# Optimization experiments

Hardware: AMD Instinct MI355X
Metric: run time of the kernel (lower is better)

## Reference

```python
import jax, jax.numpy as jnp
import numpy as np

D_MODEL = 2048
NUM_HEADS = 16
D_HEAD = D_MODEL // NUM_HEADS
ROPE_THETA = 10000.0
MAX_SEQ_LEN = 2048
NEG_INF = -1e30


def _rope_tables(seq_len):
    pos = jnp.arange(seq_len, dtype=jnp.float32)[:, None]          # [s,1]
    i = jnp.arange(0, D_HEAD, 2, dtype=jnp.float32)                 # [d/2]
    freqs = 1.0 / (ROPE_THETA ** (i / D_HEAD))
    angles = pos * freqs                                            # [s, d/2]
    return jnp.cos(angles), jnp.sin(angles)


def _apply_rope(x, cos, sin):
    # x: [b,h,s,d]; interleaved pairs: x1 = even dims, x2 = odd dims
    x1 = x[..., 0::2]
    x2 = x[..., 1::2]
    r1 = x1 * cos - x2 * sin
    r2 = x1 * sin + x2 * cos
    return jnp.stack([r1, r2], axis=-1).reshape(x.shape)


def setup_inputs() -> dict:
    key = jax.random.key(0)
    ks = jax.random.split(key, 5)
    b, s = 2, 2048
    scale = 1.0 / np.sqrt(D_MODEL)  # ~kaiming fan_in scale
    return {
        "x": jax.random.normal(ks[0], (b, s, D_MODEL), jnp.float32),
        "Wq": jax.random.normal(ks[1], (D_MODEL, D_MODEL), jnp.float32) * scale,
        "bq": jnp.zeros((D_MODEL,), jnp.float32),
        "Wk": jax.random.normal(ks[2], (D_MODEL, D_MODEL), jnp.float32) * scale,
        "bk": jnp.zeros((D_MODEL,), jnp.float32),
        "Wv": jax.random.normal(ks[3], (D_MODEL, D_MODEL), jnp.float32) * scale,
        "bv": jnp.zeros((D_MODEL,), jnp.float32),
        "Wo": jax.random.normal(ks[4], (D_MODEL, D_MODEL), jnp.float32) * scale,
        "bo": jnp.zeros((D_MODEL,), jnp.float32),
    }


def reference(x, Wq, bq, Wk, bk, Wv, bv, Wo, bo):
    b, s, _ = x.shape
    # QKV projections (torch Linear: y = x @ W.T + b)
    q = x @ Wq.T + bq
    k = x @ Wk.T + bk
    v = x @ Wv.T + bv
    # split heads: b s (h d) -> b h s d
    def split(t):
        return t.reshape(b, s, NUM_HEADS, D_HEAD).transpose(0, 2, 1, 3)
    q, k, v = split(q), split(k), split(v)
    # RoPE
    cos, sin = _rope_tables(s)
    q = _apply_rope(q, cos, sin)
    k = _apply_rope(k, cos, sin)
    # scaled dot-product attention with causal mask
    scores = jnp.einsum('bhqd,bhkd->bhqk', q, k) / jnp.sqrt(jnp.float32(D_HEAD))
    causal = jnp.tril(jnp.ones((s, s), dtype=bool))
    scores = jnp.where(causal[None, None], scores, NEG_INF)
    attn = jax.nn.softmax(scores, axis=-1)
    out = jnp.einsum('bhqk,bhkd->bhqd', attn, v)
    # merge heads and output projection
    out = out.transpose(0, 2, 1, 3).reshape(b, s, D_MODEL)
    return out @ Wo.T + bo
```

## Files before the change

### kernel.cpp

```cpp
#include <hip/hip_runtime.h>
#include <math.h>

#define D_MODEL 2048
#define NH 16
#define DH 128
#define SEQ 2048
#define NBH 32

typedef unsigned short u16;
typedef unsigned int u32;
typedef __attribute__((ext_vector_type(8))) short short8;
typedef __attribute__((ext_vector_type(4))) float floatx4;
typedef __attribute__((ext_vector_type(4))) unsigned short ushort4v;

__device__ __forceinline__ u16 f2bf(float f) {
  u32 u = __builtin_bit_cast(u32, f);
  return (u16)((u + 0x8000u) >> 16);
}
__device__ __forceinline__ float bf2f(u16 h) {
  return __builtin_bit_cast(float, (u32)h << 16);
}

__device__ __forceinline__ void async_load16(const u16* g, u16* l) {
  __builtin_amdgcn_global_load_lds(
      (const __attribute__((address_space(1))) void*)g,
      (__attribute__((address_space(3))) void*)l, 16, 0, 0);
}

template <int CTRL>
__device__ __forceinline__ float dpp_mov(float x) {
  return __builtin_bit_cast(
      float, __builtin_amdgcn_update_dpp(0, __builtin_bit_cast(int, x), CTRL,
                                         0xf, 0xf, false));
}
__device__ __forceinline__ float rmax16(float x) {
  x = fmaxf(x, dpp_mov<0x121>(x));
  x = fmaxf(x, dpp_mov<0x122>(x));
  x = fmaxf(x, dpp_mov<0x124>(x));
  x = fmaxf(x, dpp_mov<0x128>(x));
  return x;
}
__device__ __forceinline__ float radd16(float x) {
  x += dpp_mov<0x121>(x);
  x += dpp_mov<0x122>(x);
  x += dpp_mov<0x124>(x);
  x += dpp_mov<0x128>(x);
  return x;
}

__global__ void cvt_multi(const float* __restrict__ s0, u16* __restrict__ d0,
                          const float* __restrict__ s1, u16* __restrict__ d1,
                          const float* __restrict__ s2, u16* __restrict__ d2,
                          const float* __restrict__ s3, u16* __restrict__ d3,
                          const float* __restrict__ s4, u16* __restrict__ d4,
                          int nx, int nw) {
  const float* s;
  u16* d;
  int n;
  switch (blockIdx.y) {
    case 0: s = s0; d = d0; n = nx; break;
    case 1: s = s1; d = d1; n = nw; break;
    case 2: s = s2; d = d2; n = nw; break;
    case 3: s = s3; d = d3; n = nw; break;
    default: s = s4; d = d4; n = nw; break;
  }
  const int i = (blockIdx.x * 256 + threadIdx.x) * 8;
  if (i >= n) return;
  const floatx4 a = *(const floatx4*)(s + i);
  const floatx4 b = *(const floatx4*)(s + i + 4);
  short8 h;
  h[0] = (short)f2bf(a[0]); h[1] = (short)f2bf(a[1]);
  h[2] = (short)f2bf(a[2]); h[3] = (short)f2bf(a[3]);
  h[4] = (short)f2bf(b[0]); h[5] = (short)f2bf(b[1]);
  h[6] = (short)f2bf(b[2]); h[7] = (short)f2bf(b[3]);
  *(short8*)(d + i) = h;
}

__global__ __launch_bounds__(256, 2) void gemm_async(
    const u16* __restrict__ A, const u16* __restrict__ W0,
    const u16* __restrict__ W1, const u16* __restrict__ W2,
    const float* __restrict__ b0, const float* __restrict__ b1,
    const float* __restrict__ b2, void* __restrict__ C0, void* __restrict__ C1,
    void* __restrict__ C2, const int qkv) {
  __shared__ u16 As[128 * 64];
  __shared__ u16 Bs[128 * 64];
  const int tid = threadIdx.x;
  const int wave = tid >> 6, lane = tid & 63;
  const int lr = lane & 15, lg = lane >> 4;
  const int m0 = blockIdx.y * 128;
  const int wm = (wave & 1) * 64, wn = (wave >> 1) * 64;

  int n0, mode;
  const u16* W;
  const float* bias;
  void* C;
  if (qkv) {
    const int which = blockIdx.x >> 4;
    n0 = (blockIdx.x & 15) * 128;
    W = which == 0 ? W0 : which == 1 ? W1 : W2;
    bias = which == 0 ? b0 : which == 1 ? b1 : b2;
    C = which == 0 ? C0 : which == 1 ? C1 : C2;
    mode = which;
  } else {
    n0 = blockIdx.x * 128;
    W = W0; bias = b0; C = C0; mode = 3;
  }

  floatx4 acc[4][4];
#pragma unroll
  for (int i = 0; i < 4; ++i)
#pragma unroll
    for (int j = 0; j < 4; ++j) {
      floatx4 z = {0.f, 0.f, 0.f, 0.f};
      acc[i][j] = z;
    }

  for (int kt = 0; kt < D_MODEL; kt += 64) {
#pragma unroll
    for (int p = 0; p < 4; ++p) {
      const int s = p * 256 + tid;
      const int row = s >> 3, c = s & 7;
      const int g = c ^ (row & 7);
      async_load16(A + (size_t)(m0 + row) * D_MODEL + kt + g * 8,
                   &As[(p * 256 + wave * 64) * 8]);
    }
#pragma unroll
    for (int p = 0; p < 4; ++p) {
      const int s = p * 256 + tid;
      const int row = s >> 3, c = s & 7;
      const int g = c ^ (row & 7);
      async_load16(W + (size_t)(n0 + row) * D_MODEL + kt + g * 8,
                   &Bs[(p * 256 + wave * 64) * 8]);
    }
    __syncthreads();

#pragma unroll
    for (int ks = 0; ks < 2; ++ks) {
      short8 af[4], bfr[4];
      const int ch = (ks * 4 + lg) ^ (lr & 7);
#pragma unroll
      for (int i = 0; i < 4; ++i)
        af[i] = *(const short8*)&As[(wm + 16 * i + lr) * 64 + ch * 8];
#pragma unroll
      for (int j = 0; j < 4; ++j)
        bfr[j] = *(const short8*)&Bs[(wn + 16 * j + lr) * 64 + ch * 8];
#pragma unroll
      for (int i = 0; i < 4; ++i)
#pragma unroll
        for (int j = 0; j < 4; ++j)
          acc[i][j] = __builtin_amdgcn_mfma_f32_16x16x32_bf16(af[i], bfr[j],
                                                              acc[i][j], 0, 0, 0);
    }
    __syncthreads();
  }

  float bj[4];
  int ncol[4];
#pragma unroll
  for (int j = 0; j < 4; ++j) {
    ncol[j] = n0 + wn + 16 * j + lr;
    bj[j] = bias[ncol[j]];
  }

  if (mode == 3) {
    float* Cf = (float*)C;
#pragma unroll
    for (int i = 0; i < 4; ++i)
#pragma unroll
      for (int r = 0; r < 4; ++r) {
        const int m = m0 + wm + 16 * i + lg * 4 + r;
#pragma unroll
        for (int j = 0; j < 4; ++j)
          Cf[(size_t)m * D_MODEL + ncol[j]] = acc[i][j][r] + bj[j];
      }
  } else if (mode == 2) {
    u16* Ch = (u16*)C;
#pragma unroll
    for (int i = 0; i < 4; ++i)
#pragma unroll
      for (int r = 0; r < 4; ++r) {
        const int m = m0 + wm + 16 * i + lg * 4 + r;
        const int b = m >> 11, s = m & (SEQ - 1);
#pragma unroll
        for (int j = 0; j < 4; ++j) {
          const int h = ncol[j] >> 7, d = ncol[j] & (DH - 1);
          Ch[((size_t)((b * NH + h) * DH + d)) * SEQ + s] =
              f2bf(acc[i][j][r] + bj[j]);
        }
      }
  } else {
    u16* Ch = (u16*)C;
#pragma unroll
    for (int i = 0; i < 4; ++i)
#pragma unroll
      for (int r = 0; r < 4; ++r) {
        const int m = m0 + wm + 16 * i + lg * 4 + r;
        const int b = m >> 11, s = m & (SEQ - 1);
#pragma unroll
        for (int j = 0; j < 4; ++j) {
          const int h = ncol[j] >> 7, d = ncol[j] & (DH - 1);
          Ch[((size_t)((b * NH + h) * SEQ + s)) * DH + d] =
              f2bf(acc[i][j][r] + bj[j]);
        }
      }
  }
}

__global__ void rope_kernel(u16* __restrict__ Q, u16* __restrict__ K) {
  const int idx = blockIdx.x * blockDim.x + threadIdx.x;
  const int p = idx & 63;
  const int s = (idx >> 6) & (SEQ - 1);
  const int bh = idx >> 17;
  if (bh >= NBH) return;
  const float freq = exp2f(-(float)p * (13.287712379549449f / 64.0f));
  const float ang = (float)s * freq;
  float sn, cs;
  sincosf(ang, &sn, &cs);
  const size_t base = ((size_t)bh * SEQ + s) * DH + 2 * p;
  {
    const u32 qq = *(const u32*)(Q + base);
    const float x1 = bf2f((u16)(qq & 0xffffu)), x2 = bf2f((u16)(qq >> 16));
    *(u32*)(Q + base) =
        (u32)f2bf(x1 * cs - x2 * sn) | ((u32)f2bf(x1 * sn + x2 * cs) << 16);
  }
  {
    const u32 kk = *(const u32*)(K + base);
    const float x1 = bf2f((u16)(kk & 0xffffu)), x2 = bf2f((u16)(kk >> 16));
    *(u32*)(K + base) =
        (u32)f2bf(x1 * cs - x2 * sn) | ((u32)f2bf(x1 * sn + x2 * cs) << 16);
  }
}

__global__ __launch_bounds__(512, 4) void attn_kernel(
    const u16* __restrict__ Q, const u16* __restrict__ K,
    const u16* __restrict__ Vt, u16* __restrict__ Oflat) {
  __shared__ u16 Ks[64 * 128];
  __shared__ u16 Vts[128 * 64];
  __shared__ u16 Ps[8 * 16 * 72];
  const int tid = threadIdx.x;
  const int wave = tid >> 6, lane = tid & 63;
  const int lr = lane & 15, lg = lane >> 4;
  const int bh = blockIdx.y;
  const int qt = (blockIdx.y < 16) ? blockIdx.x : (15 - blockIdx.x);
  const size_t qk0 = (size_t)bh * SEQ * DH;
  const int q0 = qt * 128 + wave * 16;
  const float SL2E = 0.08838834764831845f * 1.4426950408889634f;

  short8 qf[4];
#pragma unroll
  for (int kb = 0; kb < 4; ++kb)
    qf[kb] = *(const short8*)(Q + qk0 + (size_t)(q0 + lr) * DH + kb * 32 + lg * 8);

  floatx4 o[8];
#pragma unroll
  for (int jd = 0; jd < 8; ++jd) {
    floatx4 z = {0.f, 0.f, 0.f, 0.f};
    o[jd] = z;
  }
  float mrun[4], lrun[4];
#pragma unroll
  for (int r = 0; r < 4; ++r) {
    mrun[r] = -1e38f;
    lrun[r] = 0.f;
  }

  u16* myP = &Ps[wave * 16 * 72];
  const int nkt = 2 * qt + 2;
  for (int kt = 0; kt < nkt; ++kt) {
#pragma unroll
    for (int p = 0; p < 2; ++p) {
      const int s = p * 512 + tid;
      const int row = s >> 4, c = s & 15;
      const int g = c ^ (row & 15);
      async_load16(K + qk0 + (size_t)(kt * 64 + row) * DH + g * 8,
                   &Ks[(p * 512 + wave * 64) * 8]);
    }
#pragma unroll
    for (int p = 0; p < 2; ++p) {
      const int s = p * 512 + tid;
      const int row = s >> 3, c = s & 7;
      const int g = c ^ (row & 7);
      async_load16(Vt + (size_t)bh * DH * SEQ + (size_t)row * SEQ + kt * 64 + g * 8,
                   &Vts[(p * 512 + wave * 64) * 8]);
    }
    __syncthreads();

    floatx4 sacc[4];
#pragma unroll
    for (int j = 0; j < 4; ++j) {
      floatx4 z = {0.f, 0.f, 0.f, 0.f};
      sacc[j] = z;
    }
#pragma unroll
    for (int kb = 0; kb < 4; ++kb) {
      short8 kf[4];
#pragma unroll
      for (int j = 0; j < 4; ++j)
        kf[j] = *(const short8*)&Ks[(16 * j + lr) * 128 + ((kb * 4 + lg) ^ lr) * 8];
#pragma unroll
      for (int j = 0; j < 4; ++j)
        sacc[j] = __builtin_amdgcn_mfma_f32_16x16x32_bf16(qf[kb], kf[j],
                                                          sacc[j], 0, 0, 0);
    }

    const bool mask_tile = (kt >= 2 * qt);
#pragma unroll
    for (int j = 0; j < 4; ++j)
#pragma unroll
      for (int r = 0; r < 4; ++r) {
        float v = sacc[j][r] * SL2E;
        if (mask_tile) {
          const int kpos = kt * 64 + 16 * j + lr;
          const int qpos = q0 + lg * 4 + r;
          if (kpos > qpos) v = -1e30f;
        }
        sacc[j][r] = v;
      }

    float mnew[4], alpha[4], rs[4];
#pragma unroll
    for (int r = 0; r < 4; ++r) {
      float mx = fmaxf(fmaxf(sacc[0][r], sacc[1][r]),
                       fmaxf(sacc[2][r], sacc[3][r]));
      mx = rmax16(mx);
      const float mn = fmaxf(mrun[r], mx);
      mnew[r] = mn;
      alpha[r] = exp2f(mrun[r] - mn);
      mrun[r] = mn;
      rs[r] = 0.f;
    }

#pragma unroll
    for (int j = 0; j < 4; ++j)
#pragma unroll
      for (int r = 0; r < 4; ++r) {
        const float pv = exp2f(sacc[j][r] - mnew[r]);
        rs[r] += pv;
        myP[(lg * 4 + r) * 72 + 16 * j + lr] = f2bf(pv);
      }

#pragma unroll
    for (int r = 0; r < 4; ++r)
      lrun[r] = lrun[r] * alpha[r] + radd16(rs[r]);

#pragma unroll
    for (int jd = 0; jd < 8; ++jd)
#pragma unroll
      for (int r = 0; r < 4; ++r) o[jd][r] *= alpha[r];

    asm volatile("s_waitcnt lgkmcnt(0)" ::: "memory");

#pragma unroll
    for (int kb = 0; kb < 2; ++kb) {
      const short8 pf = *(const short8*)&myP[lr * 72 + kb * 32 + lg * 8];
#pragma unroll
      for (int jd = 0; jd < 8; ++jd) {
        const short8 vf = *(const short8*)&Vts[(16 * jd + lr) * 64 +
                                               ((kb * 4 + lg) ^ (lr & 7)) * 8];
        o[jd] = __builtin_amdgcn_mfma_f32_16x16x32_bf16(pf, vf, o[jd], 0, 0, 0);
      }
    }
    __syncthreads();
  }

  const int b = bh >> 4, h = bh & (NH - 1);
#pragma unroll
  for (int r = 0; r < 4; ++r) {
    const int qpos = q0 + lg * 4 + r;
    const float inv = 1.0f / lrun[r];
    u16* dst = Oflat + ((size_t)(b * SEQ + qpos)) * D_MODEL + h * DH;
#pragma unroll
    for (int jd = 0; jd < 8; ++jd) dst[16 * jd + lr] = f2bf(o[jd][r] * inv);
  }
}

template <int ABF16>
__global__ __launch_bounds__(256, 2) void gemm_kernel(
    const void* __restrict__ Aptr, const float* __restrict__ W,
    const float* __restrict__ bias, void* __restrict__ Cptr, const int mode) {
  __shared__ u16 As[128 * 72];
  __shared__ u16 Bs[128 * 72];
  const int tid = threadIdx.x;
  const int wave = tid >> 6, lane = tid & 63;
  const int lr = lane & 15, lg = lane >> 4;
  const int m0 = blockIdx.y * 128, n0 = blockIdx.x * 128;
  const int wm = (wave & 1) * 64, wn = (wave >> 1) * 64;

  floatx4 acc[4][4];
#pragma unroll
  for (int i = 0; i < 4; ++i)
#pragma unroll
    for (int j = 0; j < 4; ++j) {
      floatx4 z = {0.f, 0.f, 0.f, 0.f};
      acc[i][j] = z;
    }

  for (int kt = 0; kt < D_MODEL; kt += 64) {
    if (ABF16) {
      const u16* A = (const u16*)Aptr;
      const int row0 = tid >> 3, c8 = (tid & 7) * 8;
#pragma unroll
      for (int p = 0; p < 4; ++p) {
        const int row = row0 + p * 32;
        *(short8*)&As[row * 72 + c8] =
            *(const short8*)(A + (size_t)(m0 + row) * D_MODEL + kt + c8);
      }
    } else {
      const float* A = (const float*)Aptr;
      const int row0 = tid >> 4, c4 = (tid & 15) * 4;
#pragma unroll
      for (int p = 0; p < 8; ++p) {
        const int row = row0 + p * 16;
        const floatx4 v =
            *(const floatx4*)(A + (size_t)(m0 + row) * D_MODEL + kt + c4);
        ushort4v h;
        h[0] = f2bf(v[0]); h[1] = f2bf(v[1]); h[2] = f2bf(v[2]); h[3] = f2bf(v[3]);
        *(ushort4v*)&As[row * 72 + c4] = h;
      }
    }
    {
      const int row0 = tid >> 4, c4 = (tid & 15) * 4;
#pragma unroll
      for (int p = 0; p < 8; ++p) {
        const int row = row0 + p * 16;
        const floatx4 v =
            *(const floatx4*)(W + (size_t)(n0 + row) * D_MODEL + kt + c4);
        ushort4v h;
        h[0] = f2bf(v[0]); h[1] = f2bf(v[1]); h[2] = f2bf(v[2]); h[3] = f2bf(v[3]);
        *(ushort4v*)&Bs[row * 72 + c4] = h;
      }
    }
    __syncthreads();
#pragma unroll
    for (int ks = 0; ks < 2; ++ks) {
      short8 af[4], bfr[4];
#pragma unroll
      for (int i = 0; i < 4; ++i)
        af[i] = *(const short8*)&As[(wm + 16 * i + lr) * 72 + ks * 32 + lg * 8];
#pragma unroll
      for (int j = 0; j < 4; ++j)
        bfr[j] = *(const short8*)&Bs[(wn + 16 * j + lr) * 72 + ks * 32 + lg * 8];
#pragma unroll
      for (int i = 0; i < 4; ++i)
#pragma unroll
        for (int j = 0; j < 4; ++j)
          acc[i][j] = __builtin_amdgcn_mfma_f32_16x16x32_bf16(af[i], bfr[j],
                                                              acc[i][j], 0, 0, 0);
    }
    __syncthreads();
  }

  float bj[4];
  int ncol[4];
#pragma unroll
  for (int j = 0; j < 4; ++j) {
    ncol[j] = n0 + wn + 16 * j + lr;
    bj[j] = bias[ncol[j]];
  }

  if (mode == 3) {
    float* C = (float*)Cptr;
#pragma unroll
    for (int i = 0; i < 4; ++i)
#pragma unroll
      for (int r = 0; r < 4; ++r) {
        const int m = m0 + wm + 16 * i + lg * 4 + r;
#pragma unroll
        for (int j = 0; j < 4; ++j)
          C[(size_t)m * D_MODEL + ncol[j]] = acc[i][j][r] + bj[j];
      }
  } else if (mode == 2) {
    u16* C = (u16*)Cptr;
#pragma unroll
    for (int i = 0; i < 4; ++i)
#pragma unroll
      for (int r = 0; r < 4; ++r) {
        const int m = m0 + wm + 16 * i + lg * 4 + r;
        const int b = m >> 11, s = m & (SEQ - 1);
#pragma unroll
        for (int j = 0; j < 4; ++j) {
          const int h = ncol[j] >> 7, d = ncol[j] & (DH - 1);
          C[((size_t)((b * NH + h) * DH + d)) * SEQ + s] = f2bf(acc[i][j][r] + bj[j]);
        }
      }
  } else {
    u16* C = (u16*)Cptr;
#pragma unroll
    for (int i = 0; i < 4; ++i)
#pragma unroll
      for (int r = 0; r < 4; ++r) {
        const int m = m0 + wm + 16 * i + lg * 4 + r;
        const int b = m >> 11, s = m & (SEQ - 1);
#pragma unroll
        for (int j = 0; j < 4; ++j) {
          const int h = ncol[j] >> 7, d = ncol[j] & (DH - 1);
          C[((size_t)((b * NH + h) * SEQ + s)) * DH + d] = f2bf(acc[i][j][r] + bj[j]);
        }
      }
  }
}

extern "C" void kernel_launch(void* const* d_in, const int* in_sizes, int n_in,
                              void* d_out, int out_size, void* d_ws,
                              size_t ws_size, hipStream_t stream) {
  const float* x = (const float*)d_in[0];
  const float* Wq = (const float*)d_in[1];
  const float* bq = (const float*)d_in[2];
  const float* Wk = (const float*)d_in[3];
  const float* bk = (const float*)d_in[4];
  const float* Wv = (const float*)d_in[5];
  const float* bv = (const float*)d_in[6];
  const float* Wo = (const float*)d_in[7];
  const float* bo = (const float*)d_in[8];
  float* out = (float*)d_out;

  const size_t E = (size_t)NBH * SEQ * DH;
  const size_t WE = (size_t)D_MODEL * D_MODEL;
  const size_t need = (4 * E + 4 * WE) * sizeof(u16);

  const dim3 gb(256);

  if (ws_size >= need) {
    u16* xb = (u16*)d_ws;
    u16* wqb = xb + E;
    u16* wkb = wqb + WE;
    u16* wvb = wkb + WE;
    u16* wob = wvb + WE;
    u16* q = wob + WE;
    u16* k = q + E;
    u16* vt = k + E;
    u16* aflat = xb;

    cvt_multi<<<dim3((int)(E / 2048), 5), gb, 0, stream>>>(
        x, xb, Wq, wqb, Wk, wkb, Wv, wvb, Wo, wob, (int)E, (int)WE);

    gemm_async<<<dim3(48, 32), gb, 0, stream>>>(xb, wqb, wkb, wvb, bq, bk, bv,
                                                q, k, vt, 1);
    rope_kernel<<<dim3((NBH * SEQ * (DH / 2)) / 256), gb, 0, stream>>>(q, k);
    attn_kernel<<<dim3(SEQ / 128, NBH), dim3(512), 0, stream>>>(q, k, vt, aflat);
    gemm_async<<<dim3(16, 32), gb, 0, stream>>>(aflat, wob, nullptr, nullptr,
                                                bo, nullptr, nullptr, out,
                                                nullptr, nullptr, 0);
  } else {
    u16* q = (u16*)d_ws;
    u16* k = q + E;
    u16* vt = k + E;
    u16* aflat = vt + E;
    const dim3 gg(D_MODEL / 128, (2 * SEQ) / 128);
    gemm_kernel<0><<<gg, gb, 0, stream>>>(x, Wq, bq, q, 0);
    gemm_kernel<0><<<gg, gb, 0, stream>>>(x, Wk, bk, k, 1);
    gemm_kernel<0><<<gg, gb, 0, stream>>>(x, Wv, bv, vt, 2);
    rope_kernel<<<dim3((NBH * SEQ * (DH / 2)) / 256), dim3(256), 0, stream>>>(q, k);
    attn_kernel<<<dim3(SEQ / 128, NBH), dim3(512), 0, stream>>>(q, k, vt, aflat);
    gemm_kernel<1><<<gg, gb, 0, stream>>>(aflat, Wo, bo, out, 3);
  }
}
```

Baseline: 417.2 us.

## Double-buffer shared tiles in QKV GEMM and attention to overlap loads

The QKV/output GEMM and the attention kernel now keep two shared-memory buffers and prefetch the next K-tile while computing on the current one, with one barrier per iteration instead of two. In attention, the probability tile reuses the consumed K buffer with an XOR swizzle, so extra LDS is avoided and an extra barrier is placed after QK. RoPE switches to the fast __sincosf intrinsic. The cost is double the LDS in the GEMM, which may reduce occupancy, and lower sincos accuracy at large angles.

```diff
diff --git a/kernel.cpp b/kernel.cpp
--- a/kernel.cpp
+++ b/kernel.cpp
@@ -82,8 +82,8 @@
     const float* __restrict__ b0, const float* __restrict__ b1,
     const float* __restrict__ b2, void* __restrict__ C0, void* __restrict__ C1,
     void* __restrict__ C2, const int qkv) {
-  __shared__ u16 As[128 * 64];
-  __shared__ u16 Bs[128 * 64];
+  __shared__ u16 As[2][128 * 64];
+  __shared__ u16 Bs[2][128 * 64];
   const int tid = threadIdx.x;
   const int wave = tid >> 6, lane = tid & 63;
   const int lr = lane & 15, lg = lane >> 4;
@@ -106,23 +106,14 @@
     W = W0; bias = b0; C = C0; mode = 3;
   }
 
-  floatx4 acc[4][4];
-#pragma unroll
-  for (int i = 0; i < 4; ++i)
-#pragma unroll
-    for (int j = 0; j < 4; ++j) {
-      floatx4 z = {0.f, 0.f, 0.f, 0.f};
-      acc[i][j] = z;
-    }
-
-  for (int kt = 0; kt < D_MODEL; kt += 64) {
+  auto stage = [&](int kt, int bsel) {
 #pragma unroll
     for (int p = 0; p < 4; ++p) {
       const int s = p * 256 + tid;
       const int row = s >> 3, c = s & 7;
       const int g = c ^ (row & 7);
       async_load16(A + (size_t)(m0 + row) * D_MODEL + kt + g * 8,
-                   &As[(p * 256 + wave * 64) * 8]);
+                   &As[bsel][(p * 256 + wave * 64) * 8]);
     }
 #pragma unroll
     for (int p = 0; p < 4; ++p) {
@@ -130,9 +121,24 @@
       const int row = s >> 3, c = s & 7;
       const int g = c ^ (row & 7);
       async_load16(W + (size_t)(n0 + row) * D_MODEL + kt + g * 8,
-                   &Bs[(p * 256 + wave * 64) * 8]);
-    }
+                   &Bs[bsel][(p * 256 + wave * 64) * 8]);
+    }
+  };
+
+  floatx4 acc[4][4];
+#pragma unroll
+  for (int i = 0; i < 4; ++i)
+#pragma unroll
+    for (int j = 0; j < 4; ++j) {
+      floatx4 z = {0.f, 0.f, 0.f, 0.f};
+      acc[i][j] = z;
+    }
+
+  stage(0, 0);
+  for (int it = 0; it < 32; ++it) {
+    const int cur = it & 1;
     __syncthreads();
+    if (it < 31) stage((it + 1) * 64, cur ^ 1);
 
 #pragma unroll
     for (int ks = 0; ks < 2; ++ks) {
@@ -140,10 +146,10 @@
       const int ch = (ks * 4 + lg) ^ (lr & 7);
 #pragma unroll
       for (int i = 0; i < 4; ++i)
-        af[i] = *(const short8*)&As[(wm + 16 * i + lr) * 64 + ch * 8];
+        af[i] = *(const short8*)&As[cur][(wm + 16 * i + lr) * 64 + ch * 8];
 #pragma unroll
       for (int j = 0; j < 4; ++j)
-        bfr[j] = *(const short8*)&Bs[(wn + 16 * j + lr) * 64 + ch * 8];
+        bfr[j] = *(const short8*)&Bs[cur][(wn + 16 * j + lr) * 64 + ch * 8];
 #pragma unroll
       for (int i = 0; i < 4; ++i)
 #pragma unroll
@@ -151,7 +157,6 @@
           acc[i][j] = __builtin_amdgcn_mfma_f32_16x16x32_bf16(af[i], bfr[j],
                                                               acc[i][j], 0, 0, 0);
     }
-    __syncthreads();
   }
 
   float bj[4];
@@ -215,7 +220,7 @@
   const float freq = exp2f(-(float)p * (13.287712379549449f / 64.0f));
   const float ang = (float)s * freq;
   float sn, cs;
-  sincosf(ang, &sn, &cs);
+  __sincosf(ang, &sn, &cs);
   const size_t base = ((size_t)bh * SEQ + s) * DH + 2 * p;
   {
     const u32 qq = *(const u32*)(Q + base);
@@ -234,9 +239,8 @@
 __global__ __launch_bounds__(512, 4) void attn_kernel(
     const u16* __restrict__ Q, const u16* __restrict__ K,
     const u16* __restrict__ Vt, u16* __restrict__ Oflat) {
-  __shared__ u16 Ks[64 * 128];
-  __shared__ u16 Vts[128 * 64];
-  __shared__ u16 Ps[8 * 16 * 72];
+  __shared__ u16 Ks[2][64 * 128];
+  __shared__ u16 Vts[2][128 * 64];
   const int tid = threadIdx.x;
   const int wave = tid >> 6, lane = tid & 63;
   const int lr = lane & 15, lg = lane >> 4;
@@ -246,44 +250,56 @@
   const int q0 = qt * 128 + wave * 16;
   const float SL2E = 0.08838834764831845f * 1.4426950408889634f;
 
-  short8 qf[4];
-#pragma unroll
-  for (int kb = 0; kb < 4; ++kb)
-    qf[kb] = *(const short8*)(Q + qk0 + (size_t)(q0 + lr) * DH + kb * 32 + lg * 8);
-
-  floatx4 o[8];
-#pragma unroll
-  for (int jd = 0; jd < 8; ++jd) {
-    floatx4 z = {0.f, 0.f, 0.f, 0.f};
-    o[jd] = z;
-  }
-  float mrun[4], lrun[4];
-#pragma unroll
-  for (int r = 0; r < 4; ++r) {
-    mrun[r] = -1e38f;
-    lrun[r] = 0.f;
-  }
-
-  u16* myP = &Ps[wave * 16 * 72];
-  const int nkt = 2 * qt + 2;
-  for (int kt = 0; kt < nkt; ++kt) {
+  auto stage_k = [&](int kt, int b) {
 #pragma unroll
     for (int p = 0; p < 2; ++p) {
       const int s = p * 512 + tid;
       const int row = s >> 4, c = s & 15;
       const int g = c ^ (row & 15);
       async_load16(K + qk0 + (size_t)(kt * 64 + row) * DH + g * 8,
-                   &Ks[(p * 512 + wave * 64) * 8]);
-    }
+                   &Ks[b][(p * 512 + wave * 64) * 8]);
+    }
+  };
+  auto stage_v = [&](int kt, int b) {
 #pragma unroll
     for (int p = 0; p < 2; ++p) {
       const int s = p * 512 + tid;
       const int row = s >> 3, c = s & 7;
       const int g = c ^ (row & 7);
-      async_load16(Vt + (size_t)bh * DH * SEQ + (size_t)row * SEQ + kt * 64 + g * 8,
-                   &Vts[(p * 512 + wave * 64) * 8]);
-    }
+      async_load16(
+          Vt + (size_t)bh * DH * SEQ + (size_t)row * SEQ + kt * 64 + g * 8,
+          &Vts[b][(p * 512 + wave * 64) * 8]);
+    }
+  };
+
+  short8 qf[4];
+#pragma unroll
+  for (int kb = 0; kb < 4; ++kb)
+    qf[kb] = *(const short8*)(Q + qk0 + (size_t)(q0 + lr) * DH + kb * 32 + lg * 8);
+
+  floatx4 o[8];
+#pragma unroll
+  for (int jd = 0; jd < 8; ++jd) {
+    floatx4 z = {0.f, 0.f, 0.f, 0.f};
+    o[jd] = z;
+  }
+  float mrun[4], lrun[4];
+#pragma unroll
+  for (int r = 0; r < 4; ++r) {
+    mrun[r] = -1e38f;
+    lrun[r] = 0.f;
+  }
+
+  const int nkt = 2 * qt + 2;
+  stage_k(0, 0);
+  stage_v(0, 0);
+  for (int kt = 0; kt < nkt; ++kt) {
+    const int cur = kt & 1;
     __syncthreads();
+    if (kt + 1 < nkt) {
+      stage_k(kt + 1, cur ^ 1);
+      stage_v(kt + 1, cur ^ 1);
+    }
 
     floatx4 sacc[4];
 #pragma unroll
@@ -296,12 +312,16 @@
       short8 kf[4];
 #pragma unroll
       for (int j = 0; j < 4; ++j)
-        kf[j] = *(const short8*)&Ks[(16 * j + lr) * 128 + ((kb * 4 + lg) ^ lr) * 8];
+        kf[j] =
+            *(const short8*)&Ks[cur][(16 * j + lr) * 128 + ((kb * 4 + lg) ^ lr) * 8];
 #pragma unroll
       for (int j = 0; j < 4; ++j)
         sacc[j] = __builtin_amdgcn_mfma_f32_16x16x32_bf16(qf[kb], kf[j],
                                                           sacc[j], 0, 0, 0);
     }
+
+    asm volatile("s_waitcnt lgkmcnt(0)\n\ts_barrier" ::: "memory");
+    u16* myP = &Ks[cur][wave * 1024];
 
     const bool mask_tile = (kt >= 2 * qt);
 #pragma unroll
@@ -336,7 +356,9 @@
       for (int r = 0; r < 4; ++r) {
         const float pv = exp2f(sacc[j][r] - mnew[r]);
         rs[r] += pv;
-        myP[(lg * 4 + r) * 72 + 16 * j + lr] = f2bf(pv);
+        const int row = lg * 4 + r;
+        myP[row * 64 + ((2 * j + (lr >> 3)) ^ (row & 7)) * 8 + (lr & 7)] =
+            f2bf(pv);
       }
 
 #pragma unroll
@@ -352,15 +374,15 @@
 
 #pragma unroll
     for (int kb = 0; kb < 2; ++kb) {
-      const short8 pf = *(const short8*)&myP[lr * 72 + kb * 32 + lg * 8];
+      const short8 pf =
+          *(const short8*)&myP[lr * 64 + ((kb * 4 + lg) ^ (lr & 7)) * 8];
 #pragma unroll
       for (int jd = 0; jd < 8; ++jd) {
-        const short8 vf = *(const short8*)&Vts[(16 * jd + lr) * 64 +
-                                               ((kb * 4 + lg) ^ (lr & 7)) * 8];
+        const short8 vf = *(const short8*)&Vts[cur][(16 * jd + lr) * 64 +
+                                                    ((kb * 4 + lg) ^ (lr & 7)) * 8];
         o[jd] = __builtin_amdgcn_mfma_f32_16x16x32_bf16(pf, vf, o[jd], 0, 0, 0);
       }
     }
-    __syncthreads();
   }
 
   const int b = bh >> 4, h = bh & (NH - 1);
```

New measurement: 457.9 us. +9.7%, slower.

## Shrink attention query tile to 64 rows with 4 waves and swizzled P buffer

Applied to the files above, without the earlier changes.

The attention kernel now uses 256-thread blocks covering 64 query rows instead of 512 threads covering 128. This halves the K/V tile reuse per block but gives finer causal work granularity, twice as many blocks, and only one masked diagonal tile per block. The P scratch buffer moves from padded rows to an XOR-swizzled layout to avoid LDS bank conflicts. RoPE also switches to the fast __sincosf intrinsic, which is less accurate for large angles.

```diff
diff --git a/kernel.cpp b/kernel.cpp
--- a/kernel.cpp
+++ b/kernel.cpp
@@ -215,7 +215,7 @@
   const float freq = exp2f(-(float)p * (13.287712379549449f / 64.0f));
   const float ang = (float)s * freq;
   float sn, cs;
-  sincosf(ang, &sn, &cs);
+  __sincosf(ang, &sn, &cs);
   const size_t base = ((size_t)bh * SEQ + s) * DH + 2 * p;
   {
     const u32 qq = *(const u32*)(Q + base);
@@ -231,19 +231,19 @@
   }
 }
 
-__global__ __launch_bounds__(512, 4) void attn_kernel(
+__global__ __launch_bounds__(256, 4) void attn_kernel(
     const u16* __restrict__ Q, const u16* __restrict__ K,
     const u16* __restrict__ Vt, u16* __restrict__ Oflat) {
   __shared__ u16 Ks[64 * 128];
   __shared__ u16 Vts[128 * 64];
-  __shared__ u16 Ps[8 * 16 * 72];
+  __shared__ u16 Ps[4 * 16 * 64];
   const int tid = threadIdx.x;
   const int wave = tid >> 6, lane = tid & 63;
   const int lr = lane & 15, lg = lane >> 4;
   const int bh = blockIdx.y;
-  const int qt = (blockIdx.y < 16) ? blockIdx.x : (15 - blockIdx.x);
+  const int qt = (bh < 16) ? blockIdx.x : (31 - blockIdx.x);
   const size_t qk0 = (size_t)bh * SEQ * DH;
-  const int q0 = qt * 128 + wave * 16;
+  const int q0 = qt * 64 + wave * 16;
   const float SL2E = 0.08838834764831845f * 1.4426950408889634f;
 
   short8 qf[4];
@@ -264,24 +264,25 @@
     lrun[r] = 0.f;
   }
 
-  u16* myP = &Ps[wave * 16 * 72];
-  const int nkt = 2 * qt + 2;
+  u16* myP = &Ps[wave * 1024];
+  const int nkt = qt + 1;
   for (int kt = 0; kt < nkt; ++kt) {
 #pragma unroll
-    for (int p = 0; p < 2; ++p) {
-      const int s = p * 512 + tid;
+    for (int p = 0; p < 4; ++p) {
+      const int s = p * 256 + tid;
       const int row = s >> 4, c = s & 15;
       const int g = c ^ (row & 15);
       async_load16(K + qk0 + (size_t)(kt * 64 + row) * DH + g * 8,
-                   &Ks[(p * 512 + wave * 64) * 8]);
-    }
-#pragma unroll
-    for (int p = 0; p < 2; ++p) {
-      const int s = p * 512 + tid;
+                   &Ks[(p * 256 + wave * 64) * 8]);
+    }
+#pragma unroll
+    for (int p = 0; p < 4; ++p) {
+      const int s = p * 256 + tid;
       const int row = s >> 3, c = s & 7;
       const int g = c ^ (row & 7);
-      async_load16(Vt + (size_t)bh * DH * SEQ + (size_t)row * SEQ + kt * 64 + g * 8,
-                   &Vts[(p * 512 + wave * 64) * 8]);
+      async_load16(
+          Vt + (size_t)bh * DH * SEQ + (size_t)row * SEQ + kt * 64 + g * 8,
+          &Vts[(p * 256 + wave * 64) * 8]);
     }
     __syncthreads();
 
@@ -303,19 +304,22 @@
                                                           sacc[j], 0, 0, 0);
     }
 
-    const bool mask_tile = (kt >= 2 * qt);
-#pragma unroll
-    for (int j = 0; j < 4; ++j)
-#pragma unroll
-      for (int r = 0; r < 4; ++r) {
-        float v = sacc[j][r] * SL2E;
-        if (mask_tile) {
+    if (kt == qt) {
+#pragma unroll
+      for (int j = 0; j < 4; ++j)
+#pragma unroll
+        for (int r = 0; r < 4; ++r) {
+          float v = sacc[j][r] * SL2E;
           const int kpos = kt * 64 + 16 * j + lr;
           const int qpos = q0 + lg * 4 + r;
-          if (kpos > qpos) v = -1e30f;
+          sacc[j][r] = (kpos > qpos) ? -1e30f : v;
         }
-        sacc[j][r] = v;
-      }
+    } else {
+#pragma unroll
+      for (int j = 0; j < 4; ++j)
+#pragma unroll
+        for (int r = 0; r < 4; ++r) sacc[j][r] *= SL2E;
+    }
 
     float mnew[4], alpha[4], rs[4];
 #pragma unroll
@@ -336,7 +340,9 @@
       for (int r = 0; r < 4; ++r) {
         const float pv = exp2f(sacc[j][r] - mnew[r]);
         rs[r] += pv;
-        myP[(lg * 4 + r) * 72 + 16 * j + lr] = f2bf(pv);
+        const int row = lg * 4 + r;
+        myP[row * 64 + ((2 * j + (lr >> 3)) ^ (row & 7)) * 8 + (lr & 7)] =
+            f2bf(pv);
       }
 
 #pragma unroll
@@ -352,7 +358,8 @@
 
 #pragma unroll
     for (int kb = 0; kb < 2; ++kb) {
-      const short8 pf = *(const short8*)&myP[lr * 72 + kb * 32 + lg * 8];
+      const short8 pf =
+          *(const short8*)&myP[lr * 64 + ((kb * 4 + lg) ^ (lr & 7)) * 8];
 #pragma unroll
       for (int jd = 0; jd < 8; ++jd) {
         const short8 vf = *(const short8*)&Vts[(16 * jd + lr) * 64 +
@@ -537,7 +544,7 @@
     gemm_async<<<dim3(48, 32), gb, 0, stream>>>(xb, wqb, wkb, wvb, bq, bk, bv,
                                                 q, k, vt, 1);
     rope_kernel<<<dim3((NBH * SEQ * (DH / 2)) / 256), gb, 0, stream>>>(q, k);
-    attn_kernel<<<dim3(SEQ / 128, NBH), dim3(512), 0, stream>>>(q, k, vt, aflat);
+    attn_kernel<<<dim3(SEQ / 64, NBH), gb, 0, stream>>>(q, k, vt, aflat);
     gemm_async<<<dim3(16, 32), gb, 0, stream>>>(aflat, wob, nullptr, nullptr,
                                                 bo, nullptr, nullptr, out,
                                                 nullptr, nullptr, 0);
@@ -551,7 +558,7 @@
     gemm_kernel<0><<<gg, gb, 0, stream>>>(x, Wk, bk, k, 1);
     gemm_kernel<0><<<gg, gb, 0, stream>>>(x, Wv, bv, vt, 2);
     rope_kernel<<<dim3((NBH * SEQ * (DH / 2)) / 256), dim3(256), 0, stream>>>(q, k);
-    attn_kernel<<<dim3(SEQ / 128, NBH), dim3(512), 0, stream>>>(q, k, vt, aflat);
+    attn_kernel<<<dim3(SEQ / 64, NBH), gb, 0, stream>>>(q, k, vt, aflat);
     gemm_kernel<1><<<gg, gb, 0, stream>>>(aflat, Wo, bo, out, 3);
   }
 }
```

Measured after the change: 425.1 us. About the same (+1.9%).
